# Performance work log

Hardware: AMD Instinct MI355X
Metric: run time of the kernel (lower is better)

## Reference

```python
import jax, jax.numpy as jnp
import numpy as np

T, B, D, H, A = 256, 512, 128, 128, 8
RUN_COUNT = 1000

def _orth(k, shape, scale):
    w = jax.random.normal(k, shape, jnp.float32)
    q, r = jnp.linalg.qr(w)
    q = q * jnp.sign(jnp.diag(r))[None, :]
    return scale * q

def setup_inputs() -> dict:
    key = jax.random.key(0)
    ks = jax.random.split(key, 12)
    return {
        'hidden': jnp.zeros((B, H), jnp.float32),
        'obs': jax.random.normal(ks[0], (T, B, D), jnp.float32),
        'dones': (jax.random.randint(ks[1], (T, B), 0, 10) == 0),
        'mean_obs': jax.random.normal(ks[2], (D,), jnp.float32) * 0.1,
        'welford_S': jax.random.uniform(ks[3], (D,), jnp.float32) * RUN_COUNT,
        'running_count': RUN_COUNT,
        'W_emb': _orth(ks[4], (D, H), float(np.sqrt(2.0))), 'b_emb': jnp.zeros((H,), jnp.float32),
        'Wi': jax.random.normal(ks[5], (H, 3 * H), jnp.float32) / np.sqrt(H),
        'Wh': jax.random.normal(ks[6], (H, 3 * H), jnp.float32) / np.sqrt(H),
        'bh': jnp.zeros((3 * H,), jnp.float32),
        'W_act': _orth(ks[7], (H, H), 2.0), 'b_act': jnp.zeros((H,), jnp.float32),
        'W_alpha': _orth(ks[8], (H, A), 0.01), 'b_alpha': jnp.zeros((A,), jnp.float32),
        'W_beta': _orth(ks[9], (H, A), 0.01), 'b_beta': jnp.zeros((A,), jnp.float32),
    }

def _welford(M0, S0, count0, xs):
    # sequential Welford update over stacked rows, as in the original lax.scan
    def step(carry, x):
        M, S, c = carry
        c = c + 1.0
        M_new = M + (x - M) / c
        S_new = S + (x - M) * (x - M_new)
        return (M_new, S_new, c), None
    (M, S, c), _ = jax.lax.scan(step, (M0, S0, jnp.asarray(count0, jnp.float32)), xs)
    return M, S, c

def reference(hidden, obs, dones, mean_obs, welford_S, running_count,
              W_emb, b_emb, Wi, Wh, bh, W_act, b_act, W_alpha, b_alpha, W_beta, b_beta):
    # --- running-stat normalization (running_count > 0 branch) ---
    stacked = obs.reshape(-1, obs.shape[-1])  # [T*B, D]
    M, S, c = _welford(mean_obs, welford_S, running_count, stacked)
    var = S / (c - 1.0)
    obs_n = (obs - M) / (jnp.sqrt(var) + 1e-8)
    # --- embedding MLP ---
    emb = jax.nn.relu(obs_n @ W_emb + b_emb)  # [T, B, H]
    # --- GRU scan over time; precompute input-side gate projections (no input bias, flax GRUCell) ---
    xg = emb @ Wi  # [T, B, 3H]
    def gru_step(h, inp):
        x3, reset = inp
        h = jnp.where(reset[:, None], 0.0, h)  # reset carry where done
        hg = h @ Wh + bh
        xr, xz, xn = jnp.split(x3, 3, axis=-1)
        hr, hz, hn = jnp.split(hg, 3, axis=-1)
        r = jax.nn.sigmoid(xr + hr)
        z = jax.nn.sigmoid(xz + hz)
        n = jnp.tanh(xn + r * hn)
        h_new = (1.0 - z) * n + z * h
        return h_new, h_new
    h_last, ys = jax.lax.scan(gru_step, hidden, (xg, dones))  # ys: [T, B, H]
    # --- policy heads ---
    act = jax.nn.relu(ys @ W_act + b_act)
    alpha = jax.nn.softplus(act @ W_alpha + b_alpha) + 1.0
    beta = jax.nn.softplus(act @ W_beta + b_beta) + 1.0
    return h_last, alpha, beta, M, S
```

## Files before the change

### kernel.cpp

```cpp
#include <hip/hip_runtime.h>

#define T_DIM 256
#define B_DIM 512
#define D_DIM 128
#define H_DIM 128
#define A_DIM 8
#define N_ROWS (T_DIM*B_DIM)
#define NT (N_ROWS/16)
#define NWIN 16
#define WLEN 16
#define LOG2E 1.4426950408889634f

typedef __attribute__((ext_vector_type(4))) float f32x4;
typedef __attribute__((ext_vector_type(8))) short bf16x8;
typedef __attribute__((ext_vector_type(4))) short bf16x4;
typedef __attribute__((ext_vector_type(8))) _Float16 f16x8;
typedef __attribute__((ext_vector_type(4))) unsigned u32x4;
typedef __attribute__((ext_vector_type(2))) unsigned u32x2;

#define OFF_PSUM   0ull
#define OFF_PSQ    1048576ull
#define OFF_STATM  2097152ull
#define OFF_STATI  2097664ull
#define OFF_WEMB   2098176ull
#define OFF_WI     2130944ull
#define OFF_WH     2229248ull
#define OFF_WACT   2425856ull
#define OFF_WHEAD  2458624ull
#define OFF_TLO    2462720ull
#define OFF_UH     2464768ull
#define OFF_XG     4194304ull
#define OFF_YS     104857600ull

#define OUT_H      0
#define OUT_ALPHA  65536
#define OUT_BETA   1114112
#define OUT_M      2162688
#define OUT_S      2162816

__device__ inline short f2bf(float x){
  union { float f; unsigned u; } v; v.f = x;
  unsigned r = v.u + 0x7FFFu + ((v.u>>16)&1u);
  return (short)(r>>16);
}
__device__ inline float bf2f(short h){
  union { unsigned u; float f; } v; v.u = ((unsigned)(unsigned short)h)<<16; return v.f;
}

__device__ inline int swz(int row, int col){ return row*136 + col; }

__device__ inline unsigned cvtpk_bf16(float lo, float hi){
  unsigned r;
  asm("v_cvt_pk_bf16_f32 %0, %1, %2" : "=v"(r) : "v"(lo), "v"(hi));
  return r;
}

__global__ __launch_bounds__(256) void k_partial(const float* __restrict__ obs,
                                                 double* __restrict__ psum,
                                                 double* __restrict__ psq){
  int tid = threadIdx.x; int col = tid & 127; int rh = tid >> 7;
  double s = 0.0, q = 0.0;
  for (int r = blockIdx.x*2 + rh; r < N_ROWS; r += 2048){
    float v = obs[(size_t)r*D_DIM + col];
    s += (double)v; q += (double)v*(double)v;
  }
  __shared__ double ls[256], lq[256];
  ls[tid]=s; lq[tid]=q; __syncthreads();
  if (rh==0){
    psum[(size_t)blockIdx.x*128 + col] = ls[tid] + ls[tid+128];
    psq [(size_t)blockIdx.x*128 + col] = lq[tid] + lq[tid+128];
  }
}

__global__ __launch_bounds__(1024) void k_stats(const double* __restrict__ psum,
                                                const double* __restrict__ psq,
                                                const float* __restrict__ mean_obs,
                                                const float* __restrict__ welfS,
                                                const int* __restrict__ runcnt,
                                                float* __restrict__ outM, float* __restrict__ outS,
                                                float* __restrict__ wsM,  float* __restrict__ wsI){
  int tid = threadIdx.x; int col = tid & 127; int seg = tid >> 7;
  double s=0.0, q=0.0;
  for (int b=seg; b<1024; b+=8){ s += psum[(size_t)b*128+col]; q += psq[(size_t)b*128+col]; }
  __shared__ double ls[1024], lq[1024];
  ls[tid]=s; lq[tid]=q; __syncthreads();
  if (seg==0){
    for (int b=1;b<8;b++){ s += ls[b*128+col]; q += lq[b*128+col]; }
    double c0 = (double)runcnt[0];
    double Nn = (double)N_ROWS;
    double n  = c0 + Nn;
    double M0 = (double)mean_obs[col], S0 = (double)welfS[col];
    double mb = s / Nn;
    double delta = mb - M0;
    double M = M0 + delta * Nn / n;
    double M2b = q - Nn*mb*mb;
    double S = S0 + M2b + delta*delta*c0*Nn/n;
    double var = S / (n - 1.0);
    float inv = (float)(1.0/(sqrt(var)+1e-8));
    outM[col] = (float)M; outS[col] = (float)S;
    wsM[col]  = (float)M; wsI[col]  = inv;
  }
}

__global__ void k_pack_all(const float* __restrict__ W_emb, const float* __restrict__ Wi,
                           const float* __restrict__ Wh,    const float* __restrict__ W_act,
                           const float* __restrict__ W_al,  const float* __restrict__ W_be,
                           short* __restrict__ Bemb, short* __restrict__ BWi,
                           short* __restrict__ BWh,  short* __restrict__ Bact,
                           short* __restrict__ Bhead){
  int gidx = blockIdx.x*256 + threadIdx.x;
  if (gidx >= 133120) return;
  if (gidx >= 131072){
    int idx = gidx - 131072;
    int j = idx & 7, lane = (idx>>3)&63, kb = (idx>>9)&3;
    int k = kb*32 + (lane>>4)*8 + j;
    int n = lane & 15;
    float wv = (n<8) ? W_al[(size_t)k*8 + n] : W_be[(size_t)k*8 + (n-8)];
    Bhead[idx] = f2bf(wv);
    return;
  }
  const float* src; short* dst; int C; int fmt; int idx;
  if (gidx < 16384)      { src=W_emb; dst=Bemb; C=128; fmt=0; idx=gidx; }
  else if (gidx < 65536) { src=Wi;    dst=BWi;  C=384; fmt=0; idx=gidx-16384; }
  else if (gidx < 114688){ src=Wh;    dst=BWh;  C=384; fmt=1; idx=gidx-65536; }
  else                   { src=W_act; dst=Bact; C=128; fmt=0; idx=gidx-114688; }
  int j = idx & 7, lane = (idx>>3)&63, kb = (idx>>9)&3, ct = idx>>11;
  int k = kb*32 + (lane>>4)*8 + j;
  int n = ct*16 + (lane&15);
  float wv = src[(size_t)k*C + n];
  short h;
  if (fmt==0) h = f2bf(wv);
  else {
    wv *= (n < 256) ? LOG2E : (2.f*LOG2E);
    union { _Float16 hf; short s; } u; u.hf = (_Float16)wv; h = u.s;
  }
  dst[idx] = h;
}

__global__ __launch_bounds__(512) void k_sched(const unsigned char* __restrict__ dones,
                                               int* __restrict__ tlo,
                                               unsigned char* __restrict__ usehid){
  int k = blockIdx.x;
  int b = threadIdx.x;
  int t0 = 0, uh = 1;
  if (k > 0){
    for (int t = WLEN*k; t >= 0; t--){
      if (dones[(size_t)t*B_DIM + b]){ t0 = t; uh = 0; break; }
    }
  }
  usehid[k*B_DIM + b] = (unsigned char)uh;
  __shared__ int red[512];
  red[b] = t0; __syncthreads();
  if (b < 32){
    int m = red[b*16];
    #pragma unroll
    for (int i=1;i<16;i++) m = min(m, red[b*16+i]);
    tlo[k*32 + b] = m;
  }
}

__global__ __launch_bounds__(512) void k_embxg(const float* __restrict__ obs,
                                               const float* __restrict__ wsM,
                                               const float* __restrict__ wsI,
                                               const short* __restrict__ Bemb,
                                               const float* __restrict__ b_emb,
                                               const short* __restrict__ BWi,
                                               const float* __restrict__ bh,
                                               short* __restrict__ xgpk){
  int tid=threadIdx.x, w=tid>>6, lane=tid&63, q=lane>>4, l=lane&15;
  int rt = blockIdx.x;
  int r0 = rt*16;
  __shared__ __align__(16) short obsL[16*136];
  __shared__ __align__(16) short embL[16*136];

  {
    int row = tid>>5, seg = tid&31;
    f32x4 o = *(const f32x4*)(obs + (size_t)(r0+row)*D_DIM + seg*4);
    f32x4 m = *(const f32x4*)(wsM + seg*4);
    f32x4 iv= *(const f32x4*)(wsI + seg*4);
    bf16x4 v;
    v[0]=f2bf((o[0]-m[0])*iv[0]); v[1]=f2bf((o[1]-m[1])*iv[1]);
    v[2]=f2bf((o[2]-m[2])*iv[2]); v[3]=f2bf((o[3]-m[3])*iv[3]);
    *(bf16x4*)&obsL[swz(row, seg*4)] = v;
  }
  __syncthreads();

  bf16x8 A[4];
  #pragma unroll
  for (int kb=0;kb<4;kb++) A[kb] = *(const bf16x8*)&obsL[swz(l, kb*32+q*8)];

  const bf16x8* BE = (const bf16x8*)Bemb;
  f32x4 accE = {0.f,0.f,0.f,0.f};
  #pragma unroll
  for (int kb=0;kb<4;kb++)
    accE = __builtin_amdgcn_mfma_f32_16x16x32_bf16(A[kb], BE[(w*4+kb)*64+lane], accE, 0,0,0);
  {
    float bb = b_emb[w*16 + l];
    #pragma unroll
    for (int r2=0;r2<4;r2++){
      float e = accE[r2] + bb; e = e>0.f ? e : 0.f;
      int b = q*4+r2;
      embL[swz(b, w*16+l)] = f2bf(e);
    }
  }
  __syncthreads();

  bf16x8 A2[4];
  #pragma unroll
  for (int kb=0;kb<4;kb++) A2[kb] = *(const bf16x8*)&embL[swz(l, kb*32+q*8)];

  const bf16x8* BW = (const bf16x8*)BWi;
  u32x2* xg8 = (u32x2*)xgpk;
  #pragma unroll
  for (int g=0; g<3; g++){
    int ct = g*8 + w;
    f32x4 acc = {0.f,0.f,0.f,0.f};
    #pragma unroll
    for (int kb=0;kb<4;kb++)
      acc = __builtin_amdgcn_mfma_f32_16x16x32_bf16(A2[kb], BW[(ct*4+kb)*64+lane], acc, 0,0,0);
    int col = ct*16 + l;
    float bb = (g<2) ? bh[col] : 0.f;
    float sc = (g<2) ? LOG2E : (2.f*LOG2E);
    u32x2 pv;
    pv[0] = cvtpk_bf16((acc[0]+bb)*sc, (acc[1]+bb)*sc);
    pv[1] = cvtpk_bf16((acc[2]+bb)*sc, (acc[3]+bb)*sc);
    xg8[((size_t)rt*24 + ct)*64 + lane] = pv;
  }
}

#define LDB(g,kb) __builtin_bit_cast(f16x8, pw4[(((g)*8+w)*4+(kb))*64+lane])
__global__
__attribute__((amdgpu_flat_work_group_size(512,512)))
__attribute__((amdgpu_waves_per_eu(4,4)))
void k_gru(const float* __restrict__ hidden,
           const unsigned char* __restrict__ dones,
           const short* __restrict__ xgpk,
           const short* __restrict__ BWh,
           const float* __restrict__ bh,
           const int* __restrict__ tlo,
           const unsigned char* __restrict__ usehid,
           short* __restrict__ yspk,
           float* __restrict__ h_last){
  int tid=threadIdx.x, w=tid>>6, lane=tid&63, q=lane>>4, l=lane&15;
  int kk = blockIdx.x >> 5, bt = blockIdx.x & 31;
  int t_out0 = kk*WLEN;
  int t_end  = t_out0 + WLEN;
  int t_start = tlo[kk*32 + bt];

  __shared__ __align__(16) _Float16 hF[2][16*136];

  const u32x4* pw4 = (const u32x4*)BWh;
  f16x8 B00 = LDB(0,0), B01 = LDB(0,1), B02 = LDB(0,2), B03 = LDB(0,3);
  f16x8 B10 = LDB(1,0), B11 = LDB(1,1), B12 = LDB(1,2), B13 = LDB(1,3);
  f16x8 B20 = LDB(2,0), B21 = LDB(2,1), B22 = LDB(2,2), B23 = LDB(2,3);

  float bh2c = bh[2*128 + w*16 + l] * (2.f*LOG2E);

  float hv[4];
  #pragma unroll
  for (int r2=0;r2<4;r2++){
    int b = bt*16 + q*4 + r2;
    hv[r2] = usehid[kk*B_DIM + b] ? hidden[(size_t)b*H_DIM + w*16 + l] : 0.f;
  }

  const bf16x4* xgt = (const bf16x4*)xgpk + (((size_t)t_start*32 + bt)*24 + w)*64 + lane;
  const unsigned char* dnp = dones + (size_t)t_start*B_DIM + bt*16 + q*4;
  bf16x4* yst = (bf16x4*)yspk + (((size_t)t_start*32 + bt)*8 + w)*64 + lane;

  bf16x4 xr_c = xgt[0], xz_c = xgt[512], xn_c = xgt[1024];
  unsigned dn_c = *(const unsigned*)dnp;
  { int a1 = (t_start+1 < t_end) ? 1 : 0; xgt += (size_t)a1*49152; dnp += a1*B_DIM; }
  bf16x4 xr_n = xgt[0], xz_n = xgt[512], xn_n = xgt[1024];
  unsigned dn_n = *(const unsigned*)dnp;

  _Float16* hA = &hF[0][0];
  _Float16* hB = &hF[1][0];
  const int wo = q*4*136 + w*16 + l;
  const int ro = l*136 + q*8;

  for (int t = t_start; t < t_end; t++){
    #pragma unroll
    for (int r2=0;r2<4;r2++){
      float hvv = ((dn_c >> (r2*8)) & 255u) ? 0.f : hv[r2];
      hv[r2] = hvv;
      hA[wo + r2*136] = (_Float16)hvv;
    }
    asm volatile("s_waitcnt lgkmcnt(0)" ::: "memory");
    __builtin_amdgcn_s_barrier();
    asm volatile("" ::: "memory");

    int a2 = (t+2 < t_end) ? 1 : 0;
    xgt += (size_t)a2 * 49152;
    dnp += a2 * B_DIM;
    bf16x4 xr_2 = xgt[0], xz_2 = xgt[512], xn_2 = xgt[1024];
    unsigned dn_2 = *(const unsigned*)dnp;

    f16x8 A0 = *(const f16x8*)(hA + ro +  0);
    f16x8 A1 = *(const f16x8*)(hA + ro + 32);
    f16x8 A2 = *(const f16x8*)(hA + ro + 64);
    f16x8 A3 = *(const f16x8*)(hA + ro + 96);

    __builtin_amdgcn_s_setprio(1);
    f32x4 acc0 = {0.f,0.f,0.f,0.f}, acc1 = {0.f,0.f,0.f,0.f}, acc2 = {0.f,0.f,0.f,0.f};
    acc0 = __builtin_amdgcn_mfma_f32_16x16x32_f16(A0, B00, acc0, 0,0,0);
    acc1 = __builtin_amdgcn_mfma_f32_16x16x32_f16(A0, B10, acc1, 0,0,0);
    acc2 = __builtin_amdgcn_mfma_f32_16x16x32_f16(A0, B20, acc2, 0,0,0);
    acc0 = __builtin_amdgcn_mfma_f32_16x16x32_f16(A1, B01, acc0, 0,0,0);
    acc1 = __builtin_amdgcn_mfma_f32_16x16x32_f16(A1, B11, acc1, 0,0,0);
    acc2 = __builtin_amdgcn_mfma_f32_16x16x32_f16(A1, B21, acc2, 0,0,0);
    acc0 = __builtin_amdgcn_mfma_f32_16x16x32_f16(A2, B02, acc0, 0,0,0);
    acc1 = __builtin_amdgcn_mfma_f32_16x16x32_f16(A2, B12, acc1, 0,0,0);
    acc2 = __builtin_amdgcn_mfma_f32_16x16x32_f16(A2, B22, acc2, 0,0,0);
    acc0 = __builtin_amdgcn_mfma_f32_16x16x32_f16(A3, B03, acc0, 0,0,0);
    acc1 = __builtin_amdgcn_mfma_f32_16x16x32_f16(A3, B13, acc1, 0,0,0);
    acc2 = __builtin_amdgcn_mfma_f32_16x16x32_f16(A3, B23, acc2, 0,0,0);
    __builtin_amdgcn_s_setprio(0);

    #pragma unroll
    for (int r2=0;r2<4;r2++){
      float xr = bf2f(xr_c[r2]), xz = bf2f(xz_c[r2]), xn = bf2f(xn_c[r2]);
      float rg = __builtin_amdgcn_rcpf(1.f + __builtin_amdgcn_exp2f(-(xr + acc0[r2])));
      float zg = __builtin_amdgcn_rcpf(1.f + __builtin_amdgcn_exp2f(-(xz + acc1[r2])));
      float e2 = __builtin_amdgcn_exp2f(xn + rg*(acc2[r2] + bh2c));
      float ng = 1.f - 2.f*__builtin_amdgcn_rcpf(e2 + 1.f);
      hv[r2] = ng + zg*(hv[r2] - ng);
    }
    if (t >= t_out0){
      u32x2 pv;
      pv[0] = cvtpk_bf16(hv[0], hv[1]);
      pv[1] = cvtpk_bf16(hv[2], hv[3]);
      *(u32x2*)yst = pv;
    }
    yst += 16384;
    xr_c = xr_n; xz_c = xz_n; xn_c = xn_n; dn_c = dn_n;
    xr_n = xr_2; xz_n = xz_2; xn_n = xn_2; dn_n = dn_2;
    _Float16* tmp = hA; hA = hB; hB = tmp;
  }

  if (kk == NWIN-1){
    #pragma unroll
    for (int r2=0;r2<4;r2++)
      h_last[(size_t)(bt*16+q*4+r2)*H_DIM + w*16 + l] = hv[r2];
  }
}

__global__ __launch_bounds__(256) void k_heads(const short* __restrict__ yspk,
                                               const short* __restrict__ Bact,
                                               const float* __restrict__ b_act,
                                               const short* __restrict__ Bhead,
                                               const float* __restrict__ b_alpha,
                                               const float* __restrict__ b_beta,
                                               float* __restrict__ alpha,
                                               float* __restrict__ beta){
  int tid=threadIdx.x, w=tid>>6, lane=tid&63, q=lane>>4, l=lane&15;
  size_t rt = (size_t)blockIdx.x*4 + w;
  __shared__ __align__(16) short tl[4][16*136];
  const bf16x4* ys4 = (const bf16x4*)yspk;
  #pragma unroll
  for (int ct=0; ct<8; ct++){
    bf16x4 v = ys4[(rt*8+ct)*64+lane];
    #pragma unroll
    for (int r2=0;r2<4;r2++){ int b=q*4+r2; tl[w][swz(b, ct*16+l)] = v[r2]; }
  }
  __syncthreads();
  bf16x8 A[4];
  #pragma unroll
  for (int kb=0;kb<4;kb++) A[kb] = *(const bf16x8*)&tl[w][swz(l, kb*32+q*8)];
  __syncthreads();
  const bf16x8* BA = (const bf16x8*)Bact;
  f32x4 accA[8];
  #pragma unroll
  for (int ct=0;ct<8;ct++){ f32x4 z = {0.f,0.f,0.f,0.f}; accA[ct]=z; }
  #pragma unroll
  for (int ct=0;ct<8;ct++)
    #pragma unroll
    for (int kb=0;kb<4;kb++)
      accA[ct] = __builtin_amdgcn_mfma_f32_16x16x32_bf16(A[kb], BA[(ct*4+kb)*64+lane], accA[ct], 0,0,0);
  #pragma unroll
  for (int ct=0;ct<8;ct++){
    int col = ct*16 + l;
    float bb = b_act[col];
    #pragma unroll
    for (int r2=0;r2<4;r2++){
      float e = accA[ct][r2] + bb; e = e>0.f ? e : 0.f;
      int b = q*4+r2;
      tl[w][swz(b, col)] = f2bf(e);
    }
  }
  __syncthreads();
  bf16x8 A2[4];
  #pragma unroll
  for (int kb=0;kb<4;kb++) A2[kb] = *(const bf16x8*)&tl[w][swz(l, kb*32+q*8)];
  const bf16x8* BHd = (const bf16x8*)Bhead;
  f32x4 acc = {0.f,0.f,0.f,0.f};
  #pragma unroll
  for (int kb=0;kb<4;kb++)
    acc = __builtin_amdgcn_mfma_f32_16x16x32_bf16(A2[kb], BHd[kb*64+lane], acc, 0,0,0);
  float bb = (l<8) ? b_alpha[l] : b_beta[l-8];
  float* dst = (l<8) ? alpha : beta;
  int cc = (l<8) ? l : l-8;
  #pragma unroll
  for (int r2=0;r2<4;r2++){
    float u = acc[r2] + bb;
    float e = __builtin_amdgcn_exp2f(-fabsf(u)*LOG2E);
    float sp = fmaxf(u,0.f) + 0.6931471805599453f*__builtin_amdgcn_logf(1.f + e);
    dst[(rt*16 + q*4 + r2)*8 + cc] = sp + 1.f;
  }
}

extern "C" void kernel_launch(void* const* d_in, const int* in_sizes, int n_in,
                              void* d_out, int out_size, void* d_ws, size_t ws_size,
                              hipStream_t stream){
  const float* hidden   = (const float*)d_in[0];
  const float* obs      = (const float*)d_in[1];
  const unsigned char* dones = (const unsigned char*)d_in[2];
  const float* mean_obs = (const float*)d_in[3];
  const float* welfS    = (const float*)d_in[4];
  const int*   runcnt   = (const int*)d_in[5];
  const float* W_emb = (const float*)d_in[6];
  const float* b_emb = (const float*)d_in[7];
  const float* Wi    = (const float*)d_in[8];
  const float* Wh    = (const float*)d_in[9];
  const float* bh    = (const float*)d_in[10];
  const float* W_act = (const float*)d_in[11];
  const float* b_act = (const float*)d_in[12];
  const float* W_al  = (const float*)d_in[13];
  const float* b_al  = (const float*)d_in[14];
  const float* W_be  = (const float*)d_in[15];
  const float* b_be  = (const float*)d_in[16];
  float* out = (float*)d_out;
  char*  ws  = (char*)d_ws;

  double* psum = (double*)(ws + OFF_PSUM);
  double* psq  = (double*)(ws + OFF_PSQ);
  float*  wsM  = (float*)(ws + OFF_STATM);
  float*  wsI  = (float*)(ws + OFF_STATI);
  short*  Bemb = (short*)(ws + OFF_WEMB);
  short*  BWi  = (short*)(ws + OFF_WI);
  short*  BWh  = (short*)(ws + OFF_WH);
  short*  Bact = (short*)(ws + OFF_WACT);
  short*  Bhead= (short*)(ws + OFF_WHEAD);
  int*    tlo  = (int*)(ws + OFF_TLO);
  unsigned char* uh = (unsigned char*)(ws + OFF_UH);
  short*  xgpk = (short*)(ws + OFF_XG);
  short*  yspk = (short*)(ws + OFF_YS);

  k_partial<<<1024,256,0,stream>>>(obs, psum, psq);
  k_stats<<<1,1024,0,stream>>>(psum, psq, mean_obs, welfS, runcnt,
                               out+OUT_M, out+OUT_S, wsM, wsI);
  k_sched<<<NWIN,512,0,stream>>>(dones, tlo, uh);
  k_pack_all<<<520,256,0,stream>>>(W_emb, Wi, Wh, W_act, W_al, W_be,
                                   Bemb, BWi, BWh, Bact, Bhead);
  k_embxg<<<8192,512,0,stream>>>(obs, wsM, wsI, Bemb, b_emb, BWi, bh, xgpk);
  k_gru<<<NWIN*32,512,0,stream>>>(hidden, dones, xgpk, BWh, bh, tlo, uh,
                                  yspk, out + OUT_H);
  k_heads<<<2048,256,0,stream>>>(yspk, Bact, b_act, Bhead, b_al, b_be,
                                 out + OUT_ALPHA, out + OUT_BETA);
}
```

Baseline: 550.6 us.

## Halve GRU time windows and give each wave two hidden column tiles

Cuts the number of time windows from 16 to 32-step windows (8 windows), so there are fewer blocks and less warm-up recomputation overlap per window. Each GRU block now runs 4 waves instead of 8, and each wave computes two 16-column hidden tiles with 24 MFMAs per step, holding twice the Wh fragments in registers. This reduces barrier participants and block count but doubles the serial work per wave and lowers parallelism; with only 256 blocks, per-step latency may rise.

```diff
diff --git a/kernel.cpp b/kernel.cpp
--- a/kernel.cpp
+++ b/kernel.cpp
@@ -7,8 +7,8 @@
 #define A_DIM 8
 #define N_ROWS (T_DIM*B_DIM)
 #define NT (N_ROWS/16)
-#define NWIN 16
-#define WLEN 16
+#define NWIN 8
+#define WLEN 32
 #define LOG2E 1.4426950408889634f
 
 typedef __attribute__((ext_vector_type(4))) float f32x4;
@@ -228,10 +228,10 @@
   }
 }
 
-#define LDB(g,kb) __builtin_bit_cast(f16x8, pw4[(((g)*8+w)*4+(kb))*64+lane])
+#define LDB(g,i,kb) __builtin_bit_cast(f16x8, pw4[(((g)*8 + w*2 + (i))*4+(kb))*64+lane])
 __global__
-__attribute__((amdgpu_flat_work_group_size(512,512)))
-__attribute__((amdgpu_waves_per_eu(4,4)))
+__attribute__((amdgpu_flat_work_group_size(256,256)))
+__attribute__((amdgpu_waves_per_eu(1,1)))
 void k_gru(const float* __restrict__ hidden,
            const unsigned char* __restrict__ dones,
            const short* __restrict__ xgpk,
@@ -250,40 +250,60 @@
   __shared__ __align__(16) _Float16 hF[2][16*136];
 
   const u32x4* pw4 = (const u32x4*)BWh;
-  f16x8 B00 = LDB(0,0), B01 = LDB(0,1), B02 = LDB(0,2), B03 = LDB(0,3);
-  f16x8 B10 = LDB(1,0), B11 = LDB(1,1), B12 = LDB(1,2), B13 = LDB(1,3);
-  f16x8 B20 = LDB(2,0), B21 = LDB(2,1), B22 = LDB(2,2), B23 = LDB(2,3);
-
-  float bh2c = bh[2*128 + w*16 + l] * (2.f*LOG2E);
-
-  float hv[4];
+  f16x8 Bf[3][2][4];
+  #pragma unroll
+  for (int g=0; g<3; g++)
+    #pragma unroll
+    for (int i=0; i<2; i++)
+      #pragma unroll
+      for (int kb=0; kb<4; kb++) Bf[g][i][kb] = LDB(g,i,kb);
+
+  float bh2c[2];
+  #pragma unroll
+  for (int i=0;i<2;i++) bh2c[i] = bh[2*128 + (w*2+i)*16 + l] * (2.f*LOG2E);
+
+  float hC[2][4];
   #pragma unroll
   for (int r2=0;r2<4;r2++){
     int b = bt*16 + q*4 + r2;
-    hv[r2] = usehid[kk*B_DIM + b] ? hidden[(size_t)b*H_DIM + w*16 + l] : 0.f;
-  }
-
-  const bf16x4* xgt = (const bf16x4*)xgpk + (((size_t)t_start*32 + bt)*24 + w)*64 + lane;
+    int use = usehid[kk*B_DIM + b];
+    #pragma unroll
+    for (int i=0;i<2;i++)
+      hC[i][r2] = use ? hidden[(size_t)b*H_DIM + (w*2+i)*16 + l] : 0.f;
+  }
+
+  const bf16x4* xgt = (const bf16x4*)xgpk + (((size_t)t_start*32 + bt)*24 + w*2)*64 + lane;
   const unsigned char* dnp = dones + (size_t)t_start*B_DIM + bt*16 + q*4;
-  bf16x4* yst = (bf16x4*)yspk + (((size_t)t_start*32 + bt)*8 + w)*64 + lane;
-
-  bf16x4 xr_c = xgt[0], xz_c = xgt[512], xn_c = xgt[1024];
+  bf16x4* yst = (bf16x4*)yspk + (((size_t)t_start*32 + bt)*8 + w*2)*64 + lane;
+
+  bf16x4 xc[3][2], xn_[3][2];
+  #pragma unroll
+  for (int g=0;g<3;g++)
+    #pragma unroll
+    for (int i=0;i<2;i++) xc[g][i] = xgt[g*512 + i*64];
   unsigned dn_c = *(const unsigned*)dnp;
   { int a1 = (t_start+1 < t_end) ? 1 : 0; xgt += (size_t)a1*49152; dnp += a1*B_DIM; }
-  bf16x4 xr_n = xgt[0], xz_n = xgt[512], xn_n = xgt[1024];
+  #pragma unroll
+  for (int g=0;g<3;g++)
+    #pragma unroll
+    for (int i=0;i<2;i++) xn_[g][i] = xgt[g*512 + i*64];
   unsigned dn_n = *(const unsigned*)dnp;
 
   _Float16* hA = &hF[0][0];
   _Float16* hB = &hF[1][0];
-  const int wo = q*4*136 + w*16 + l;
   const int ro = l*136 + q*8;
 
   for (int t = t_start; t < t_end; t++){
     #pragma unroll
     for (int r2=0;r2<4;r2++){
-      float hvv = ((dn_c >> (r2*8)) & 255u) ? 0.f : hv[r2];
-      hv[r2] = hvv;
-      hA[wo + r2*136] = (_Float16)hvv;
+      int drow = (dn_c >> (r2*8)) & 255u;
+      int wrow = (q*4+r2)*136 + l;
+      #pragma unroll
+      for (int i=0;i<2;i++){
+        float hvv = drow ? 0.f : hC[i][r2];
+        hC[i][r2] = hvv;
+        hA[wrow + (w*2+i)*16] = (_Float16)hvv;
+      }
     }
     asm volatile("s_waitcnt lgkmcnt(0)" ::: "memory");
     __builtin_amdgcn_s_barrier();
@@ -292,7 +312,11 @@
     int a2 = (t+2 < t_end) ? 1 : 0;
     xgt += (size_t)a2 * 49152;
     dnp += a2 * B_DIM;
-    bf16x4 xr_2 = xgt[0], xz_2 = xgt[512], xn_2 = xgt[1024];
+    bf16x4 x2_[3][2];
+    #pragma unroll
+    for (int g=0;g<3;g++)
+      #pragma unroll
+      for (int i=0;i<2;i++) x2_[g][i] = xgt[g*512 + i*64];
     unsigned dn_2 = *(const unsigned*)dnp;
 
     f16x8 A0 = *(const f16x8*)(hA + ro +  0);
@@ -300,47 +324,54 @@
     f16x8 A2 = *(const f16x8*)(hA + ro + 64);
     f16x8 A3 = *(const f16x8*)(hA + ro + 96);
 
-    __builtin_amdgcn_s_setprio(1);
-    f32x4 acc0 = {0.f,0.f,0.f,0.f}, acc1 = {0.f,0.f,0.f,0.f}, acc2 = {0.f,0.f,0.f,0.f};
-    acc0 = __builtin_amdgcn_mfma_f32_16x16x32_f16(A0, B00, acc0, 0,0,0);
-    acc1 = __builtin_amdgcn_mfma_f32_16x16x32_f16(A0, B10, acc1, 0,0,0);
-    acc2 = __builtin_amdgcn_mfma_f32_16x16x32_f16(A0, B20, acc2, 0,0,0);
-    acc0 = __builtin_amdgcn_mfma_f32_16x16x32_f16(A1, B01, acc0, 0,0,0);
-    acc1 = __builtin_amdgcn_mfma_f32_16x16x32_f16(A1, B11, acc1, 0,0,0);
-    acc2 = __builtin_amdgcn_mfma_f32_16x16x32_f16(A1, B21, acc2, 0,0,0);
-    acc0 = __builtin_amdgcn_mfma_f32_16x16x32_f16(A2, B02, acc0, 0,0,0);
-    acc1 = __builtin_amdgcn_mfma_f32_16x16x32_f16(A2, B12, acc1, 0,0,0);
-    acc2 = __builtin_amdgcn_mfma_f32_16x16x32_f16(A2, B22, acc2, 0,0,0);
-    acc0 = __builtin_amdgcn_mfma_f32_16x16x32_f16(A3, B03, acc0, 0,0,0);
-    acc1 = __builtin_amdgcn_mfma_f32_16x16x32_f16(A3, B13, acc1, 0,0,0);
-    acc2 = __builtin_amdgcn_mfma_f32_16x16x32_f16(A3, B23, acc2, 0,0,0);
-    __builtin_amdgcn_s_setprio(0);
-
-    #pragma unroll
-    for (int r2=0;r2<4;r2++){
-      float xr = bf2f(xr_c[r2]), xz = bf2f(xz_c[r2]), xn = bf2f(xn_c[r2]);
-      float rg = __builtin_amdgcn_rcpf(1.f + __builtin_amdgcn_exp2f(-(xr + acc0[r2])));
-      float zg = __builtin_amdgcn_rcpf(1.f + __builtin_amdgcn_exp2f(-(xz + acc1[r2])));
-      float e2 = __builtin_amdgcn_exp2f(xn + rg*(acc2[r2] + bh2c));
-      float ng = 1.f - 2.f*__builtin_amdgcn_rcpf(e2 + 1.f);
-      hv[r2] = ng + zg*(hv[r2] - ng);
-    }
-    if (t >= t_out0){
-      u32x2 pv;
-      pv[0] = cvtpk_bf16(hv[0], hv[1]);
-      pv[1] = cvtpk_bf16(hv[2], hv[3]);
-      *(u32x2*)yst = pv;
+    f32x4 acc[3][2];
+    #pragma unroll
+    for (int g=0;g<3;g++)
+      #pragma unroll
+      for (int i=0;i<2;i++){ f32x4 z={0.f,0.f,0.f,0.f}; acc[g][i]=z; }
+    #pragma unroll
+    for (int g=0;g<3;g++)
+      #pragma unroll
+      for (int i=0;i<2;i++){
+        acc[g][i] = __builtin_amdgcn_mfma_f32_16x16x32_f16(A0, Bf[g][i][0], acc[g][i], 0,0,0);
+        acc[g][i] = __builtin_amdgcn_mfma_f32_16x16x32_f16(A1, Bf[g][i][1], acc[g][i], 0,0,0);
+        acc[g][i] = __builtin_amdgcn_mfma_f32_16x16x32_f16(A2, Bf[g][i][2], acc[g][i], 0,0,0);
+        acc[g][i] = __builtin_amdgcn_mfma_f32_16x16x32_f16(A3, Bf[g][i][3], acc[g][i], 0,0,0);
+      }
+
+    #pragma unroll
+    for (int i=0;i<2;i++){
+      #pragma unroll
+      for (int r2=0;r2<4;r2++){
+        float xr = bf2f(xc[0][i][r2]), xz = bf2f(xc[1][i][r2]), xn = bf2f(xc[2][i][r2]);
+        float rg = __builtin_amdgcn_rcpf(1.f + __builtin_amdgcn_exp2f(-(xr + acc[0][i][r2])));
+        float zg = __builtin_amdgcn_rcpf(1.f + __builtin_amdgcn_exp2f(-(xz + acc[1][i][r2])));
+        float e2 = __builtin_amdgcn_exp2f(xn + rg*(acc[2][i][r2] + bh2c[i]));
+        float ng = 1.f - 2.f*__builtin_amdgcn_rcpf(e2 + 1.f);
+        hC[i][r2] = ng + zg*(hC[i][r2] - ng);
+      }
+      if (t >= t_out0){
+        u32x2 pv;
+        pv[0] = cvtpk_bf16(hC[i][0], hC[i][1]);
+        pv[1] = cvtpk_bf16(hC[i][2], hC[i][3]);
+        *(u32x2*)(yst + i*64) = pv;
+      }
     }
     yst += 16384;
-    xr_c = xr_n; xz_c = xz_n; xn_c = xn_n; dn_c = dn_n;
-    xr_n = xr_2; xz_n = xz_2; xn_n = xn_2; dn_n = dn_2;
+    #pragma unroll
+    for (int g=0;g<3;g++)
+      #pragma unroll
+      for (int i=0;i<2;i++){ xc[g][i] = xn_[g][i]; xn_[g][i] = x2_[g][i]; }
+    dn_c = dn_n; dn_n = dn_2;
     _Float16* tmp = hA; hA = hB; hB = tmp;
   }
 
   if (kk == NWIN-1){
     #pragma unroll
     for (int r2=0;r2<4;r2++)
-      h_last[(size_t)(bt*16+q*4+r2)*H_DIM + w*16 + l] = hv[r2];
+      #pragma unroll
+      for (int i=0;i<2;i++)
+        h_last[(size_t)(bt*16+q*4+r2)*H_DIM + (w*2+i)*16 + l] = hC[i][r2];
   }
 }
 
@@ -452,7 +483,7 @@
   k_pack_all<<<520,256,0,stream>>>(W_emb, Wi, Wh, W_act, W_al, W_be,
                                    Bemb, BWi, BWh, Bact, Bhead);
   k_embxg<<<8192,512,0,stream>>>(obs, wsM, wsI, Bemb, b_emb, BWi, bh, xgpk);
-  k_gru<<<NWIN*32,512,0,stream>>>(hidden, dones, xgpk, BWh, bh, tlo, uh,
+  k_gru<<<NWIN*32,256,0,stream>>>(hidden, dones, xgpk, BWh, bh, tlo, uh,
                                   yspk, out + OUT_H);
   k_heads<<<2048,256,0,stream>>>(yspk, Bact, b_act, Bhead, b_al, b_be,
                                  out + OUT_ALPHA, out + OUT_BETA);
```

Measured after the change: 529.7 us. 3.8% less time.
